# Kernel tuning notes

Measured on AMD Instinct MI355X. Metric: run time of the kernel, lower is better.

Reference implementation:

```python
import jax, jax.numpy as jnp
import numpy as np

N_NODES, N_EDGES, DIM = 50000, 800000, 128


def setup_inputs() -> dict:
    key = jax.random.key(0)
    ks = jax.random.split(key, 16)
    s = 1.0 / np.sqrt(DIM)
    inp = {
        "x": jax.random.normal(ks[0], (N_NODES, DIM), dtype=jnp.float32),
        "edge_index": jax.random.randint(ks[1], (2, N_EDGES), 0, N_NODES, dtype=jnp.int64),
    }
    # 3 GIN layers, each with a 2-layer MLP (Linear-ReLU-Linear)
    for i in range(3):
        inp[f"w1_{i}"] = jax.random.normal(ks[2 + 4 * i], (DIM, DIM), dtype=jnp.float32) * s
        inp[f"b1_{i}"] = jnp.zeros((DIM,), dtype=jnp.float32)
        inp[f"w2_{i}"] = jax.random.normal(ks[3 + 4 * i], (DIM, DIM), dtype=jnp.float32) * s
        inp[f"b2_{i}"] = jnp.zeros((DIM,), dtype=jnp.float32)
    inp["wh"] = jax.random.normal(ks[14], (DIM, DIM), dtype=jnp.float32) * s
    inp["bh"] = jnp.zeros((DIM,), dtype=jnp.float32)
    return inp


def _gin_layer(h, src, dst, w1, b1, w2, b2, residual):
    # message passing: gather x[src], scatter-add at dst (aggr='sum')
    neigh = jax.ops.segment_sum(h[src], dst, num_segments=h.shape[0])
    out = h + neigh  # (1 + eps) * x + neigh, eps = 0
    out = jnp.maximum(out @ w1 + b1, 0.0) @ w2 + b2  # MLP (dropout p=0)
    if residual:  # res_fc is Identity since in_dim == out_dim
        out = out + h
    return out


def reference(x, edge_index, w1_0, b1_0, w2_0, b2_0, w1_1, b1_1, w2_1, b2_1,
              w1_2, b1_2, w2_2, b2_2, wh, bh):
    src, dst = edge_index[0], edge_index[1]
    h = x
    h = _gin_layer(h, src, dst, w1_0, b1_0, w2_0, b2_0, residual=True)
    h = _gin_layer(h, src, dst, w1_1, b1_1, w2_1, b2_1, residual=True)
    # last layer: encoding=False -> no residual
    h = _gin_layer(h, src, dst, w1_2, b1_2, w2_2, b2_2, residual=False)
    # extra_output_fc head
    return h @ wh + bh
```

## Files before the change

### kernel.cpp

```cpp
#include <hip/hip_runtime.h>
#include <hip/hip_fp16.h>

#define N_NODES 50000
#define N_EDGES 800000
#define DIM 128
#define FEAT_ELEMS (N_NODES * DIM)
#define STRIDE 64
#define NB 391
#define BCAP 3072

typedef __attribute__((ext_vector_type(8))) _Float16 f16x8;
typedef __attribute__((ext_vector_type(4))) float f32x4;
typedef __attribute__((ext_vector_type(2))) float f32x2;

#define MFMA_F16 __builtin_amdgcn_mfma_f32_16x16x32_f16


__global__ __launch_bounds__(256) void prep_combo_kernel(
    const float* __restrict__ w0, const float* __restrict__ w1,
    const float* __restrict__ w2, const float* __restrict__ w3,
    const float* __restrict__ w4, const float* __restrict__ w5,
    const float* __restrict__ w6, __half* __restrict__ dst,
    const float* __restrict__ x, __half* __restrict__ hm,
    unsigned char* __restrict__ qm, int* __restrict__ gcnt) {
    const int b = blockIdx.x;
    if (b < 112) {
        const int wsel = b >> 4;
        const int chunk = b & 15;
        const float* W;
        switch (wsel) {
            case 0: W = w0; break;
            case 1: W = w1; break;
            case 2: W = w2; break;
            case 3: W = w3; break;
            case 4: W = w4; break;
            case 5: W = w5; break;
            default: W = w6; break;
        }
        __half* d = dst + (size_t)wsel * 16384;
        int idx = chunk * 1024 + threadIdx.x;
#pragma unroll
        for (int t = 0; t < 4; ++t, idx += 256) {
            int k = idx >> 7, n = idx & 127;
            int ks = k >> 5, q = (k >> 3) & 3, j = k & 7;
            int ct = n >> 4, c = n & 15;
            int lane = q * 16 + c;
            int base = ((ks * 8 + ct) * 64 + lane) * 8 + j;
            d[base] = __float2half(W[idx]);
        }
    } else if (b < 1136) {
        int i = (b - 112) * 256 + threadIdx.x;
        const int stride = 1024 * 256;
        const int n4 = FEAT_ELEMS / 4;
        for (; i < n4; i += stride) {
            float4 v = ((const float4*)x)[i];
            __half2 h0 = __floats2half2_rn(v.x, v.y);
            __half2 h1 = __floats2half2_rn(v.z, v.w);
            uint2 u;
            u.x = *(unsigned*)&h0;
            u.y = *(unsigned*)&h1;
            ((uint2*)hm)[i] = u;
            int p = __builtin_amdgcn_cvt_pk_fp8_f32(v.x, v.y, 0, false);
            p = __builtin_amdgcn_cvt_pk_fp8_f32(v.z, v.w, p, true);
            ((int*)qm)[i] = p;
        }
    } else {
        for (int i = threadIdx.x; i < NB; i += 256) gcnt[i] = 0;
    }
}


__global__ __launch_bounds__(256) void bucket_kernel(const int* __restrict__ ei,
                                                     int* __restrict__ gcnt,
                                                     long long* __restrict__ ebuf) {
    __shared__ int hist[NB];
    __shared__ int base[NB];
    __shared__ int sh_is64;
    const int tid = threadIdx.x;
    for (int i = tid; i < NB; i += 256) hist[i] = 0;
    if (tid == 0) {
        int o = 0;
        for (int i = 1; i < 64; i += 2) o |= ei[i];
        sh_is64 = (o == 0) ? 1 : 0;
    }
    __syncthreads();
    const int e0 = blockIdx.x * 2048;
    const int is64 = sh_is64;
    int sv[8], dv[8];
    int nl = 0;
#pragma unroll
    for (int k = 0; k < 8; ++k) {
        int e = e0 + k * 256 + tid;
        if (e < N_EDGES) {
            int s = is64 ? ei[2 * e] : ei[e];
            int d = is64 ? ei[2 * (N_EDGES + e)] : ei[N_EDGES + e];
            sv[nl] = s;
            dv[nl] = d;
            atomicAdd(&hist[d >> 7], 1);
            ++nl;
        }
    }
    __syncthreads();
    for (int i = tid; i < NB; i += 256) {
        int h = hist[i];
        base[i] = h ? atomicAdd(&gcnt[i], h) : 0;
    }
    __syncthreads();
    for (int i = tid; i < NB; i += 256) hist[i] = 0;
    __syncthreads();
    for (int k = 0; k < nl; ++k) {
        int b = dv[k] >> 7;
        int r = base[b] + atomicAdd(&hist[b], 1);
        if (r < BCAP)
            ebuf[(size_t)b * BCAP + r] = ((long long)sv[k] << 32) | (unsigned)dv[k];
    }
}


__global__ __launch_bounds__(256) void build_kernel(const int* __restrict__ gcnt,
                                                    const long long* __restrict__ ebuf,
                                                    int* __restrict__ cnt,
                                                    int* __restrict__ col_idx) {
    __shared__ int cur[128];
    const int b = blockIdx.x;
    const int tid = threadIdx.x;
    if (tid < 128) cur[tid] = 0;
    __syncthreads();
    int n = gcnt[b];
    if (n > BCAP) n = BCAP;
    const long long* eb = ebuf + (size_t)b * BCAP;
    for (int i = tid; i < n; i += 256) {
        long long p = eb[i];
        int d = (int)(p & 0xFFFFFFFFll);
        int s = (int)(p >> 32);
        int slot = atomicAdd(&cur[d & 127], 1);
        if (slot < STRIDE) col_idx[d * STRIDE + slot] = s;
    }
    __syncthreads();
    int node = b * 128 + tid;
    if (tid < 128 && node < N_NODES) {
        int c = cur[tid];
        cnt[node] = (c > STRIDE) ? STRIDE : c;
    }
}


template <bool LAST>
__global__ __launch_bounds__(128, 4) void gin_layer_kernel(
    const __half* __restrict__ Hs,
    const unsigned char* __restrict__ Qm,
    const int* __restrict__ cnt,
    const int* __restrict__ col_idx,
    const __half* __restrict__ W1f,
    const __half* __restrict__ W2f,
    const __half* __restrict__ Whf,
    const float* __restrict__ b1,
    const float* __restrict__ b2,
    const float* __restrict__ bh,
    __half* __restrict__ Hout,
    unsigned char* __restrict__ Qout,
    float* __restrict__ Cout) {
    __shared__ __align__(16) __half tl[2048];
    __shared__ __align__(16) __half ul[2048];
    const int tid = threadIdx.x;
    const int lane = tid & 63;
    const int wid = tid >> 6;
    const int c = lane & 15;
    const int q = lane >> 4;
    const int R = blockIdx.x * 16;

    {
        const int g = tid >> 4;
        const int d0 = (tid & 15) * 8;
#define ACCQ(U)                                                             \
    {                                                                       \
        f32x2 g0 = __builtin_amdgcn_cvt_pk_f32_fp8((int)(U).x, false);      \
        f32x2 g1 = __builtin_amdgcn_cvt_pk_f32_fp8((int)(U).x, true);       \
        f32x2 g2 = __builtin_amdgcn_cvt_pk_f32_fp8((int)(U).y, false);      \
        f32x2 g3 = __builtin_amdgcn_cvt_pk_f32_fp8((int)(U).y, true);       \
        acc[0] += g0.x; acc[1] += g0.y; acc[2] += g1.x; acc[3] += g1.y;     \
        acc[4] += g2.x; acc[5] += g2.y; acc[6] += g3.x; acc[7] += g3.y;     \
    }
#pragma unroll
        for (int it = 0; it < 2; ++it) {
            const int rl = it * 8 + g;
            const size_t grow = (size_t)(R + rl);
            float acc[8];
            {
                uint4 sv = *(const uint4*)(Hs + grow * DIM + d0);
                const __half2* sp = (const __half2*)&sv;
                float2 s0 = __half22float2(sp[0]), s1 = __half22float2(sp[1]);
                float2 s2 = __half22float2(sp[2]), s3 = __half22float2(sp[3]);
                acc[0] = s0.x; acc[1] = s0.y; acc[2] = s1.x; acc[3] = s1.y;
                acc[4] = s2.x; acc[5] = s2.y; acc[6] = s3.x; acc[7] = s3.y;
            }
            int d = cnt[grow];
            if (d > STRIDE) d = STRIDE;
            const int* ci = col_idx + grow * STRIDE;
            int j = 0;
            for (; j + 8 <= d; j += 8) {
                int s[8];
#pragma unroll
                for (int k = 0; k < 8; ++k) s[k] = ci[j + k];
                uint2 u[8];
#pragma unroll
                for (int k = 0; k < 8; ++k)
                    u[k] = *(const uint2*)(Qm + (size_t)s[k] * DIM + d0);
#pragma unroll
                for (int k = 0; k < 8; ++k) ACCQ(u[k])
            }
            for (; j + 2 <= d; j += 2) {
                int s0 = ci[j], s1 = ci[j + 1];
                uint2 u0 = *(const uint2*)(Qm + (size_t)s0 * DIM + d0);
                uint2 u1 = *(const uint2*)(Qm + (size_t)s1 * DIM + d0);
                ACCQ(u0)
                ACCQ(u1)
            }
            if (j < d) {
                int s = ci[j];
                uint2 u = *(const uint2*)(Qm + (size_t)s * DIM + d0);
                ACCQ(u)
            }
            uint4 o;
            __half2* op = (__half2*)&o;
            op[0] = __floats2half2_rn(acc[0], acc[1]);
            op[1] = __floats2half2_rn(acc[2], acc[3]);
            op[2] = __floats2half2_rn(acc[4], acc[5]);
            op[3] = __floats2half2_rn(acc[6], acc[7]);
            *(uint4*)&tl[rl * 128 + (d0 ^ ((rl & 7) << 3))] = o;
        }
#undef ACCQ
    }
    __syncthreads();

    f16x8 a[4];
#pragma unroll
    for (int ks = 0; ks < 4; ++ks)
        a[ks] = *(const f16x8*)&tl[c * 128 + ((ks * 32 + q * 8) ^ ((c & 7) << 3))];

    f32x4 acc1[4];
#pragma unroll
    for (int t = 0; t < 4; ++t) acc1[t] = (f32x4){0.f, 0.f, 0.f, 0.f};
#pragma unroll
    for (int ks = 0; ks < 4; ++ks) {
#pragma unroll
        for (int t = 0; t < 4; ++t) {
            const int ctg = wid * 4 + t;
            f16x8 b = *(const f16x8*)(W1f + (ks * 8 + ctg) * 512 + lane * 8);
            acc1[t] = MFMA_F16(a[ks], b, acc1[t], 0, 0, 0);
        }
    }

#pragma unroll
    for (int t = 0; t < 4; ++t) {
        const int col = (wid * 4 + t) * 16 + c;
        const float bv = b1[col];
#pragma unroll
        for (int rr = 0; rr < 4; ++rr) {
            const int rl = q * 4 + rr;
            ul[rl * 128 + (col ^ ((rl & 7) << 3))] =
                __float2half(fmaxf(acc1[t][rr] + bv, 0.f));
        }
    }
    __syncthreads();

    f32x4 acc2[4];
#pragma unroll
    for (int t = 0; t < 4; ++t) acc2[t] = (f32x4){0.f, 0.f, 0.f, 0.f};
#pragma unroll
    for (int ks = 0; ks < 4; ++ks) {
        f16x8 ua = *(const f16x8*)&ul[c * 128 + ((ks * 32 + q * 8) ^ ((c & 7) << 3))];
#pragma unroll
        for (int t = 0; t < 4; ++t) {
            const int ctg = wid * 4 + t;
            f16x8 b = *(const f16x8*)(W2f + (ks * 8 + ctg) * 512 + lane * 8);
            acc2[t] = MFMA_F16(ua, b, acc2[t], 0, 0, 0);
        }
    }

#pragma unroll
    for (int t = 0; t < 4; ++t) {
        const int col = (wid * 4 + t) * 16 + c;
        const float bv = b2[col];
#pragma unroll
        for (int rr = 0; rr < 4; ++rr) {
            const int rl = q * 4 + rr;
            tl[rl * 128 + (col ^ (q << 4))] = __float2half(acc2[t][rr] + bv);
        }
    }
    __syncthreads();

    if (!LAST) {
        const int row2 = tid >> 3;
        const int cb = (tid & 7) * 8;
        const size_t grow = (size_t)(R + row2);
#pragma unroll
        for (int k = 0; k < 2; ++k) {
            const int c0 = cb + k * 64;
            uint4 hv = *(uint4*)&tl[row2 * 128 + (c0 ^ ((row2 >> 2) << 4))];
            const __half2* hp = (const __half2*)&hv;
            float2 t0 = __half22float2(hp[0]), t1 = __half22float2(hp[1]);
            float2 t2 = __half22float2(hp[2]), t3 = __half22float2(hp[3]);
            float f0 = t0.x, f1 = t0.y, f2 = t1.x, f3 = t1.y;
            float f4 = t2.x, f5 = t2.y, f6 = t3.x, f7 = t3.y;
            {
                uint4 rv = *(const uint4*)(Hs + grow * DIM + c0);
                const __half2* rp = (const __half2*)&rv;
                float2 r0 = __half22float2(rp[0]), r1 = __half22float2(rp[1]);
                float2 r2 = __half22float2(rp[2]), r3 = __half22float2(rp[3]);
                f0 += r0.x; f1 += r0.y; f2 += r1.x; f3 += r1.y;
                f4 += r2.x; f5 += r2.y; f6 += r3.x; f7 += r3.y;
            }
            uint4 ov;
            __half2* op = (__half2*)&ov;
            op[0] = __floats2half2_rn(f0, f1);
            op[1] = __floats2half2_rn(f2, f3);
            op[2] = __floats2half2_rn(f4, f5);
            op[3] = __floats2half2_rn(f6, f7);
            *(uint4*)(Hout + grow * DIM + c0) = ov;
            int q0 = __builtin_amdgcn_cvt_pk_fp8_f32(f0, f1, 0, false);
            q0 = __builtin_amdgcn_cvt_pk_fp8_f32(f2, f3, q0, true);
            int q1 = __builtin_amdgcn_cvt_pk_fp8_f32(f4, f5, 0, false);
            q1 = __builtin_amdgcn_cvt_pk_fp8_f32(f6, f7, q1, true);
            uint2 qv;
            qv.x = (unsigned)q0;
            qv.y = (unsigned)q1;
            *(uint2*)(Qout + grow * DIM + c0) = qv;
        }
    } else {
        f32x4 acc3[4];
#pragma unroll
        for (int t = 0; t < 4; ++t) acc3[t] = (f32x4){0.f, 0.f, 0.f, 0.f};
#pragma unroll
        for (int ks = 0; ks < 4; ++ks) {
            f16x8 ha =
                *(const f16x8*)&tl[c * 128 + ((ks * 32 + q * 8) ^ ((c >> 2) << 4))];
#pragma unroll
            for (int t = 0; t < 4; ++t) {
                const int ctg = wid * 4 + t;
                f16x8 b = *(const f16x8*)(Whf + (ks * 8 + ctg) * 512 + lane * 8);
                acc3[t] = MFMA_F16(ha, b, acc3[t], 0, 0, 0);
            }
        }
#pragma unroll
        for (int t = 0; t < 4; ++t) {
            const int col = (wid * 4 + t) * 16 + c;
            const float bv = bh[col];
#pragma unroll
            for (int rr = 0; rr < 4; ++rr) {
                const int row = R + q * 4 + rr;
                Cout[(size_t)row * DIM + col] = acc3[t][rr] + bv;
            }
        }
    }
}


extern "C" void kernel_launch(void* const* d_in, const int* in_sizes, int n_in,
                              void* d_out, int out_size, void* d_ws, size_t ws_size,
                              hipStream_t stream) {
    const float* x = (const float*)d_in[0];
    const int* ei = (const int*)d_in[1];
    const float* w1[3] = {(const float*)d_in[2], (const float*)d_in[6], (const float*)d_in[10]};
    const float* b1[3] = {(const float*)d_in[3], (const float*)d_in[7], (const float*)d_in[11]};
    const float* w2[3] = {(const float*)d_in[4], (const float*)d_in[8], (const float*)d_in[12]};
    const float* b2[3] = {(const float*)d_in[5], (const float*)d_in[9], (const float*)d_in[13]};
    const float* wh = (const float*)d_in[14];
    const float* bh = (const float*)d_in[15];
    float* out = (float*)d_out;

    char* ws = (char*)d_ws;
    const size_t HFEAT = (size_t)FEAT_ELEMS * sizeof(__half);
    const size_t QFEAT = (size_t)FEAT_ELEMS;
    size_t off = 0;
    int* cnt = (int*)(ws + off);                         off += 200704;
    int* col_idx = (int*)(ws + off);                     off += (size_t)N_NODES * STRIDE * 4;
    int* gcnt = (int*)(ws + off);                        off += 4096;
    __half* Wf = (__half*)(ws + off);                    off += 7 * 32768;
    long long* ebuf = (long long*)(ws + off);            off += (size_t)NB * BCAP * 8;
    __half* HMx = (__half*)(ws + off);                   off += HFEAT;
    __half* HM1 = (__half*)(ws + off);                   off += HFEAT;
    __half* HM0 = (__half*)(ws + off);                   off += HFEAT;
    unsigned char* Qx = (unsigned char*)(ws + off);      off += QFEAT;
    unsigned char* Q1 = (unsigned char*)(ws + off);      off += QFEAT;
    unsigned char* Q0 = (unsigned char*)(ws + off);      off += QFEAT;

    const int GIN_BLKS = N_NODES / 16;

    prep_combo_kernel<<<1137, 256, 0, stream>>>(w1[0], w2[0], w1[1], w2[1], w1[2], w2[2],
                                                wh, Wf, x, HMx, Qx, gcnt);
    bucket_kernel<<<NB, 256, 0, stream>>>(ei, gcnt, ebuf);
    build_kernel<<<NB, 256, 0, stream>>>(gcnt, ebuf, cnt, col_idx);

#define WF(i) (Wf + (size_t)(i) * 16384)

    gin_layer_kernel<false><<<GIN_BLKS, 128, 0, stream>>>(
        HMx, Qx, cnt, col_idx, WF(0), WF(1), nullptr, b1[0], b2[0], nullptr,
        HM1, Q1, nullptr);

    gin_layer_kernel<false><<<GIN_BLKS, 128, 0, stream>>>(
        HM1, Q1, cnt, col_idx, WF(2), WF(3), nullptr, b1[1], b2[1], nullptr,
        HM0, Q0, nullptr);

    gin_layer_kernel<true><<<GIN_BLKS, 128, 0, stream>>>(
        HM0, Q0, cnt, col_idx, WF(4), WF(5), WF(6), b1[2], b2[2], bh,
        nullptr, nullptr, out);
#undef WF
}
```

Measured before the change: 230.7 us.

## Build adjacency with direct global atomics and pad neighbor lists to multiples of eight

Replaces the two-pass bucket/build adjacency construction with a single kernel that does a global atomicAdd per edge on the destination count and writes col_idx directly. A new pad kernel rounds each node's neighbor count up to a multiple of eight and fills the extra slots with a dummy index that points at a zeroed row past the end of each FP8 feature buffer. This lets the gather loop use int4 index loads and a single unrolled eight-wide loop with no remainder handling. The costs are heavy global atomic contention on the count array and some wasted gathers of the zero row for padded slots.

```diff
diff --git a/kernel.cpp b/kernel.cpp
--- a/kernel.cpp
+++ b/kernel.cpp
@@ -6,8 +6,6 @@
 #define DIM 128
 #define FEAT_ELEMS (N_NODES * DIM)
 #define STRIDE 64
-#define NB 391
-#define BCAP 3072
 
 typedef __attribute__((ext_vector_type(8))) _Float16 f16x8;
 typedef __attribute__((ext_vector_type(4))) float f32x4;
@@ -22,7 +20,8 @@
     const float* __restrict__ w4, const float* __restrict__ w5,
     const float* __restrict__ w6, __half* __restrict__ dst,
     const float* __restrict__ x, __half* __restrict__ hm,
-    unsigned char* __restrict__ qm, int* __restrict__ gcnt) {
+    unsigned char* __restrict__ qx, unsigned char* __restrict__ q1,
+    unsigned char* __restrict__ q0, int* __restrict__ cnt) {
     const int b = blockIdx.x;
     if (b < 112) {
         const int wsel = b >> 4;
@@ -62,85 +61,50 @@
             ((uint2*)hm)[i] = u;
             int p = __builtin_amdgcn_cvt_pk_fp8_f32(v.x, v.y, 0, false);
             p = __builtin_amdgcn_cvt_pk_fp8_f32(v.z, v.w, p, true);
-            ((int*)qm)[i] = p;
+            ((int*)qx)[i] = p;
         }
     } else {
-        for (int i = threadIdx.x; i < NB; i += 256) gcnt[i] = 0;
-    }
-}
-
-
-__global__ __launch_bounds__(256) void bucket_kernel(const int* __restrict__ ei,
-                                                     int* __restrict__ gcnt,
-                                                     long long* __restrict__ ebuf) {
-    __shared__ int hist[NB];
-    __shared__ int base[NB];
+        for (int i = threadIdx.x; i < N_NODES; i += 256) cnt[i] = 0;
+        if (threadIdx.x < 32) {
+            ((unsigned*)(qx + FEAT_ELEMS))[threadIdx.x] = 0;
+            ((unsigned*)(q1 + FEAT_ELEMS))[threadIdx.x] = 0;
+            ((unsigned*)(q0 + FEAT_ELEMS))[threadIdx.x] = 0;
+        }
+    }
+}
+
+
+__global__ __launch_bounds__(256) void build_direct_kernel(const int* __restrict__ ei,
+                                                           int* __restrict__ cnt,
+                                                           int* __restrict__ col_idx) {
     __shared__ int sh_is64;
     const int tid = threadIdx.x;
-    for (int i = tid; i < NB; i += 256) hist[i] = 0;
     if (tid == 0) {
         int o = 0;
         for (int i = 1; i < 64; i += 2) o |= ei[i];
         sh_is64 = (o == 0) ? 1 : 0;
     }
     __syncthreads();
-    const int e0 = blockIdx.x * 2048;
-    const int is64 = sh_is64;
-    int sv[8], dv[8];
-    int nl = 0;
-#pragma unroll
-    for (int k = 0; k < 8; ++k) {
-        int e = e0 + k * 256 + tid;
-        if (e < N_EDGES) {
-            int s = is64 ? ei[2 * e] : ei[e];
-            int d = is64 ? ei[2 * (N_EDGES + e)] : ei[N_EDGES + e];
-            sv[nl] = s;
-            dv[nl] = d;
-            atomicAdd(&hist[d >> 7], 1);
-            ++nl;
-        }
-    }
-    __syncthreads();
-    for (int i = tid; i < NB; i += 256) {
-        int h = hist[i];
-        base[i] = h ? atomicAdd(&gcnt[i], h) : 0;
-    }
-    __syncthreads();
-    for (int i = tid; i < NB; i += 256) hist[i] = 0;
-    __syncthreads();
-    for (int k = 0; k < nl; ++k) {
-        int b = dv[k] >> 7;
-        int r = base[b] + atomicAdd(&hist[b], 1);
-        if (r < BCAP)
-            ebuf[(size_t)b * BCAP + r] = ((long long)sv[k] << 32) | (unsigned)dv[k];
-    }
-}
-
-
-__global__ __launch_bounds__(256) void build_kernel(const int* __restrict__ gcnt,
-                                                    const long long* __restrict__ ebuf,
-                                                    int* __restrict__ cnt,
-                                                    int* __restrict__ col_idx) {
-    __shared__ int cur[128];
-    const int b = blockIdx.x;
-    const int tid = threadIdx.x;
-    if (tid < 128) cur[tid] = 0;
-    __syncthreads();
-    int n = gcnt[b];
-    if (n > BCAP) n = BCAP;
-    const long long* eb = ebuf + (size_t)b * BCAP;
-    for (int i = tid; i < n; i += 256) {
-        long long p = eb[i];
-        int d = (int)(p & 0xFFFFFFFFll);
-        int s = (int)(p >> 32);
-        int slot = atomicAdd(&cur[d & 127], 1);
+    const int e = blockIdx.x * 256 + tid;
+    if (e < N_EDGES) {
+        const int is64 = sh_is64;
+        int s = is64 ? ei[2 * e] : ei[e];
+        int d = is64 ? ei[2 * (N_EDGES + e)] : ei[N_EDGES + e];
+        int slot = atomicAdd(&cnt[d], 1);
         if (slot < STRIDE) col_idx[d * STRIDE + slot] = s;
     }
-    __syncthreads();
-    int node = b * 128 + tid;
-    if (tid < 128 && node < N_NODES) {
-        int c = cur[tid];
-        cnt[node] = (c > STRIDE) ? STRIDE : c;
+}
+
+
+__global__ __launch_bounds__(256) void pad_kernel(int* __restrict__ cnt,
+                                                  int* __restrict__ col_idx) {
+    const int node = blockIdx.x * 256 + threadIdx.x;
+    if (node < N_NODES) {
+        int c = cnt[node];
+        if (c > STRIDE) c = STRIDE;
+        const int p = (c + 7) & ~7;
+        for (int s = c; s < p; ++s) col_idx[node * STRIDE + s] = N_NODES;
+        cnt[node] = p;
     }
 }
 
@@ -194,32 +158,21 @@
                 acc[0] = s0.x; acc[1] = s0.y; acc[2] = s1.x; acc[3] = s1.y;
                 acc[4] = s2.x; acc[5] = s2.y; acc[6] = s3.x; acc[7] = s3.y;
             }
-            int d = cnt[grow];
-            if (d > STRIDE) d = STRIDE;
+            const int d = cnt[grow];
             const int* ci = col_idx + grow * STRIDE;
-            int j = 0;
-            for (; j + 8 <= d; j += 8) {
-                int s[8];
-#pragma unroll
-                for (int k = 0; k < 8; ++k) s[k] = ci[j + k];
-                uint2 u[8];
-#pragma unroll
-                for (int k = 0; k < 8; ++k)
-                    u[k] = *(const uint2*)(Qm + (size_t)s[k] * DIM + d0);
-#pragma unroll
-                for (int k = 0; k < 8; ++k) ACCQ(u[k])
-            }
-            for (; j + 2 <= d; j += 2) {
-                int s0 = ci[j], s1 = ci[j + 1];
-                uint2 u0 = *(const uint2*)(Qm + (size_t)s0 * DIM + d0);
-                uint2 u1 = *(const uint2*)(Qm + (size_t)s1 * DIM + d0);
-                ACCQ(u0)
-                ACCQ(u1)
-            }
-            if (j < d) {
-                int s = ci[j];
-                uint2 u = *(const uint2*)(Qm + (size_t)s * DIM + d0);
-                ACCQ(u)
+            for (int j = 0; j < d; j += 8) {
+                int4 ia = *(const int4*)(ci + j);
+                int4 ib = *(const int4*)(ci + j + 4);
+                uint2 u0 = *(const uint2*)(Qm + (size_t)ia.x * DIM + d0);
+                uint2 u1 = *(const uint2*)(Qm + (size_t)ia.y * DIM + d0);
+                uint2 u2 = *(const uint2*)(Qm + (size_t)ia.z * DIM + d0);
+                uint2 u3 = *(const uint2*)(Qm + (size_t)ia.w * DIM + d0);
+                uint2 u4 = *(const uint2*)(Qm + (size_t)ib.x * DIM + d0);
+                uint2 u5 = *(const uint2*)(Qm + (size_t)ib.y * DIM + d0);
+                uint2 u6 = *(const uint2*)(Qm + (size_t)ib.z * DIM + d0);
+                uint2 u7 = *(const uint2*)(Qm + (size_t)ib.w * DIM + d0);
+                ACCQ(u0) ACCQ(u1) ACCQ(u2) ACCQ(u3)
+                ACCQ(u4) ACCQ(u5) ACCQ(u6) ACCQ(u7)
             }
             uint4 o;
             __half2* op = (__half2*)&o;
@@ -371,13 +324,11 @@
 
     char* ws = (char*)d_ws;
     const size_t HFEAT = (size_t)FEAT_ELEMS * sizeof(__half);
-    const size_t QFEAT = (size_t)FEAT_ELEMS;
+    const size_t QFEAT = (size_t)FEAT_ELEMS + 256;
     size_t off = 0;
     int* cnt = (int*)(ws + off);                         off += 200704;
     int* col_idx = (int*)(ws + off);                     off += (size_t)N_NODES * STRIDE * 4;
-    int* gcnt = (int*)(ws + off);                        off += 4096;
     __half* Wf = (__half*)(ws + off);                    off += 7 * 32768;
-    long long* ebuf = (long long*)(ws + off);            off += (size_t)NB * BCAP * 8;
     __half* HMx = (__half*)(ws + off);                   off += HFEAT;
     __half* HM1 = (__half*)(ws + off);                   off += HFEAT;
     __half* HM0 = (__half*)(ws + off);                   off += HFEAT;
@@ -386,11 +337,13 @@
     unsigned char* Q0 = (unsigned char*)(ws + off);      off += QFEAT;
 
     const int GIN_BLKS = N_NODES / 16;
+    const int EDGE_BLKS = (N_EDGES + 255) / 256;
+    const int NODE_BLKS = (N_NODES + 255) / 256;
 
     prep_combo_kernel<<<1137, 256, 0, stream>>>(w1[0], w2[0], w1[1], w2[1], w1[2], w2[2],
-                                                wh, Wf, x, HMx, Qx, gcnt);
-    bucket_kernel<<<NB, 256, 0, stream>>>(ei, gcnt, ebuf);
-    build_kernel<<<NB, 256, 0, stream>>>(gcnt, ebuf, cnt, col_idx);
+                                                wh, Wf, x, HMx, Qx, Q1, Q0, cnt);
+    build_direct_kernel<<<EDGE_BLKS, 256, 0, stream>>>(ei, cnt, col_idx);
+    pad_kernel<<<NODE_BLKS, 256, 0, stream>>>(cnt, col_idx);
 
 #define WF(i) (Wf + (size_t)(i) * 16384)
 
```

Result: slower. 251.6 us (+9.1%).
